# Kernel tuning notes

Hardware: AMD Instinct MI355X
Metric: run time of the kernel (lower is better)

Reference implementation:

```python
import jax, jax.numpy as jnp
import numpy as np

L, B, S, H, NH, NS = 4, 8, 2048, 1024, 2, 32
DH = H // NH


def _ln(x, g, b, eps):
    m = jnp.mean(x, axis=-1, keepdims=True)
    v = jnp.mean((x - m) ** 2, axis=-1, keepdims=True)
    return (x - m) / jnp.sqrt(v + eps) * g + b


def setup_inputs() -> dict:
    key = jax.random.key(0)
    ks = jax.random.split(key, 8)
    sc = 0.02
    hidden_states = jax.random.normal(ks[0], (L, B, S, H), jnp.float32)
    attention_mask = jnp.ones((B, S), jnp.int32)
    bnd = jnp.sort(jax.random.randint(ks[1], (B, NS + 1), 0, S - 1), axis=1)
    span_head_idxs = bnd[:, :-1]
    span_tail_idxs = jnp.maximum(bnd[:, 1:], span_head_idxs + 1)  # tail > head, <= S-... (S-1+1=S ok since slice end)
    return {
        "hidden_states": hidden_states,
        "attention_mask": attention_mask,
        "span_head_idxs": span_head_idxs,
        "span_tail_idxs": span_tail_idxs,
        "layer_weights": jnp.linspace(-5.0, 5.0, L),
        "ln1_g": jnp.ones((H,)), "ln1_b": jnp.zeros((H,)),
        "Wq": jax.random.normal(ks[2], (H, H)) * sc, "bq": jnp.zeros((H,)),
        "Wk": jax.random.normal(ks[3], (H, H)) * sc, "bk": jnp.zeros((H,)),
        "Wv": jax.random.normal(ks[4], (H, H)) * sc, "bv": jnp.zeros((H,)),
        "Wo": jax.random.normal(ks[5], (H, H)) * sc, "bo": jnp.zeros((H,)),
        "ln2_g": jnp.ones((H,)), "ln2_b": jnp.zeros((H,)),
    }


def reference(hidden_states, attention_mask, span_head_idxs, span_tail_idxs,
              layer_weights, ln1_g, ln1_b, Wq, bq, Wk, bk, Wv, bv, Wo, bo,
              ln2_g, ln2_b):
    l, b, s, h = hidden_states.shape
    # weighted layer average
    w = jax.nn.softmax(layer_weights)                      # [L]
    x = jnp.einsum('l,lbsh->bsh', w, hidden_states)        # [B,S,H]
    # extended mask (additive)
    ext = (1.0 - attention_mask.astype(x.dtype))[:, None, None, :] * -10000.0
    x = _ln(x, ln1_g, ln1_b, 1e-7)
    # BertSelfAttention (dropout = identity in eval)
    q = (x @ Wq.T + bq).reshape(b, s, NH, DH)
    k = (x @ Wk.T + bk).reshape(b, s, NH, DH)
    v = (x @ Wv.T + bv).reshape(b, s, NH, DH)
    scores = jnp.einsum('bqnd,bknd->bnqk', q, k) / jnp.sqrt(jnp.asarray(DH, x.dtype))
    probs = jax.nn.softmax(scores + ext, axis=-1)          # [B,NH,S,S]
    ctx = jnp.einsum('bnqk,bknd->bqnd', probs, v).reshape(b, s, h)
    # BertSelfOutput: dense + residual + LN (eps=1e-12 default)
    y = _ln(ctx @ Wo.T + bo + x, ln2_g, ln2_b, 1e-12)      # [B,S,H]
    # ragged per-span mean via exclusive cumsum
    csum = jnp.concatenate([jnp.zeros((b, 1, h), y.dtype), jnp.cumsum(y, axis=1)], axis=1)  # [B,S+1,H]
    sh = jnp.take_along_axis(csum, span_head_idxs[..., None], axis=1)   # [B,NS,H]
    st = jnp.take_along_axis(csum, span_tail_idxs[..., None], axis=1)
    lengths = (span_tail_idxs - span_head_idxs).astype(y.dtype)[..., None]
    return (st - sh) / lengths
```

## Files before the change

kernel.cpp:

```cpp
#include <hip/hip_runtime.h>
#include <stdint.h>

#define Ln 4
#define Bn 8
#define Sn 2048
#define Hn 1024
#define NHn 2
#define DHn 512
#define NSn 32
#define Mn (Bn*Sn)

typedef __attribute__((ext_vector_type(8))) short bf16x8;
typedef __attribute__((ext_vector_type(4))) float f32x4;
typedef unsigned short u16;

__device__ __forceinline__ float bf2f(u16 u){
  union { unsigned int i; float f; } c; c.i = ((unsigned int)u)<<16; return c.f;
}
__device__ __forceinline__ u16 f2bf(float f){
  union { float f; unsigned int i; } c; c.f = f;
  unsigned int r = c.i + 0x7FFFu + ((c.i>>16)&1u);
  return (u16)(r>>16);
}
__device__ __forceinline__ uint32_t packbf(float a, float b){
  return (uint32_t)f2bf(a) | ((uint32_t)f2bf(b)<<16);
}
__device__ __forceinline__ void gl2lds16(const void* g, void* l){
  __builtin_amdgcn_global_load_lds((const __attribute__((address_space(1))) void*)g,
                                   (__attribute__((address_space(3))) void*)l, 16, 0, 0);
}

__device__ __forceinline__ float block_sum256(float v, float* red){
#pragma unroll
  for (int m=32;m>=1;m>>=1) v += __shfl_xor(v, m, 64);
  int tid = threadIdx.x;
  if ((tid&63)==0) red[tid>>6] = v;
  __syncthreads();
  v = red[0]+red[1]+red[2]+red[3];
  __syncthreads();
  return v;
}

__global__ __launch_bounds__(256) void convw_kernel(const float* __restrict__ Wq, const float* __restrict__ Wk,
    const float* __restrict__ Wv, const float* __restrict__ Wo, u16* __restrict__ wb){
  int m = blockIdx.y;
  const float* src = (m==0)?Wq:(m==1)?Wk:(m==2)?Wv:Wo;
  size_t i = ((size_t)blockIdx.x*256 + threadIdx.x)*4;
  const float4 v = *(const float4*)&src[i];
  ushort4 o;
  o.x=f2bf(v.x); o.y=f2bf(v.y); o.z=f2bf(v.z); o.w=f2bf(v.w);
  *(ushort4*)&wb[(size_t)m*Hn*Hn + i] = o;
}

__global__ __launch_bounds__(256) void mixln_kernel(const float* __restrict__ hs, const float* __restrict__ lw,
    const float* __restrict__ g, const float* __restrict__ be, u16* __restrict__ xb){
  __shared__ float red[4];
  int row = blockIdx.x;
  int tid = threadIdx.x;
  float l0=lw[0], l1=lw[1], l2=lw[2], l3=lw[3];
  float mx = fmaxf(fmaxf(l0,l1),fmaxf(l2,l3));
  float e0=__expf(l0-mx), e1=__expf(l1-mx), e2=__expf(l2-mx), e3=__expf(l3-mx);
  float inv = 1.0f/(e0+e1+e2+e3);
  e0*=inv; e1*=inv; e2*=inv; e3*=inv;
  size_t base = (size_t)row*Hn + tid*4;
  const float4 h0 = *(const float4*)&hs[base];
  const float4 h1 = *(const float4*)&hs[base + (size_t)Mn*Hn];
  const float4 h2 = *(const float4*)&hs[base + (size_t)2*Mn*Hn];
  const float4 h3 = *(const float4*)&hs[base + (size_t)3*Mn*Hn];
  float x0 = e0*h0.x + e1*h1.x + e2*h2.x + e3*h3.x;
  float x1 = e0*h0.y + e1*h1.y + e2*h2.y + e3*h3.y;
  float x2 = e0*h0.z + e1*h1.z + e2*h2.z + e3*h3.z;
  float x3 = e0*h0.w + e1*h1.w + e2*h2.w + e3*h3.w;
  float s = block_sum256(x0+x1+x2+x3, red);
  float mean = s * (1.0f/Hn);
  float d0=x0-mean, d1=x1-mean, d2=x2-mean, d3=x3-mean;
  float sq = block_sum256(d0*d0+d1*d1+d2*d2+d3*d3, red);
  float rstd = rsqrtf(sq*(1.0f/Hn) + 1e-7f);
  int c = tid*4;
  ushort4 o;
  o.x = f2bf(d0*rstd*g[c+0] + be[c+0]);
  o.y = f2bf(d1*rstd*g[c+1] + be[c+1]);
  o.z = f2bf(d2*rstd*g[c+2] + be[c+2]);
  o.w = f2bf(d3*rstd*g[c+3] + be[c+3]);
  *(ushort4*)&xb[(size_t)row*Hn + c] = o;
}

template<int MODE>
__global__ __launch_bounds__(512,2) void gemm256_kernel(const u16* __restrict__ A, const u16* __restrict__ Bw,
    const float* __restrict__ bias, const u16* __restrict__ resid, void* __restrict__ Cout, float scale){
  __shared__ char lds[2][2][32768];
  int tid = threadIdx.x, lane = tid&63, wid = tid>>6;
  int ln = lane&15, g4 = lane>>4;
  int wm = wid>>2, wn = wid&3;
  int swz = (blockIdx.x&7)*32 + (blockIdx.x>>3);
  int i0 = (swz>>2)*256;
  int j0 = (swz&3)*256;

  f32x4 acc[8][4];
#pragma unroll
  for (int a=0;a<8;a++)
#pragma unroll
    for (int b=0;b<4;b++) acc[a][b] = (f32x4){0.f,0.f,0.f,0.f};

  const u16* Asrc = A + (size_t)i0*Hn;
  const u16* Bsrc = Bw + (size_t)j0*Hn;

#define STAGE1(SRC, DST, G) do { \
    int g_ = (G); int row_ = g_>>3; int cs_ = (g_&7) ^ (row_&7); \
    gl2lds16((SRC) + (size_t)row_*Hn + cs_*8, (DST) + g_*16); } while(0)

#define RD(BASE, ROW, KG) (*(const bf16x8*)((BASE) + (ROW)*128 + ((((KG)) ^ ((ROW)&7))<<4)))

  {
    const u16* An_ = Asrc; const u16* Bn_ = Bsrc;
#pragma unroll
    for (int c=0;c<4;++c){ STAGE1(An_, lds[0][0], tid + c*512); }
#pragma unroll
    for (int c=0;c<4;++c){ STAGE1(Bn_, lds[0][1], tid + c*512); }
  }
  __syncthreads();

  bf16x8 af[4][2], bf0[2][2], bf1[2][2];

#pragma unroll 1
  for (int t=0; t<16; ++t){
    const char* Ac = lds[t&1][0];
    const char* Bc = lds[t&1][1];
    char* Anx = lds[(t+1)&1][0];
    char* Bnx = lds[(t+1)&1][1];
    const u16* An_ = Asrc + (t+1)*64;
    const u16* Bn_ = Bsrc + (t+1)*64;
    bool st = (t < 15);
    if (st){ STAGE1(An_, Anx, tid); STAGE1(An_, Anx, tid+512); STAGE1(Bn_, Bnx, tid); }
#pragma unroll
    for (int mt=0; mt<4; ++mt)
#pragma unroll
      for (int kk=0; kk<2; ++kk) af[mt][kk] = RD(Ac, wm*128 + mt*16 + ln, kk*4+g4);
#pragma unroll
    for (int nt=0; nt<2; ++nt)
#pragma unroll
      for (int kk=0; kk<2; ++kk) bf0[nt][kk] = RD(Bc, wn*64 + nt*16 + ln, kk*4+g4);
    __builtin_amdgcn_s_barrier();
    __builtin_amdgcn_s_setprio(1);
#pragma unroll
    for (int kk=0; kk<2; ++kk)
#pragma unroll
      for (int mt=0; mt<4; ++mt)
#pragma unroll
        for (int nt=0; nt<2; ++nt)
          acc[mt][nt] = __builtin_amdgcn_mfma_f32_16x16x32_bf16(af[mt][kk], bf0[nt][kk], acc[mt][nt], 0,0,0);
    __builtin_amdgcn_s_setprio(0);
    if (st){ STAGE1(Bn_, Bnx, tid+512); STAGE1(An_, Anx, tid+1024); STAGE1(An_, Anx, tid+1536); }
#pragma unroll
    for (int nt=0; nt<2; ++nt)
#pragma unroll
      for (int kk=0; kk<2; ++kk) bf1[nt][kk] = RD(Bc, wn*64 + (2+nt)*16 + ln, kk*4+g4);
    __builtin_amdgcn_s_barrier();
    __builtin_amdgcn_s_setprio(1);
#pragma unroll
    for (int kk=0; kk<2; ++kk)
#pragma unroll
      for (int mt=0; mt<4; ++mt)
#pragma unroll
        for (int nt=0; nt<2; ++nt)
          acc[mt][2+nt] = __builtin_amdgcn_mfma_f32_16x16x32_bf16(af[mt][kk], bf1[nt][kk], acc[mt][2+nt], 0,0,0);
    __builtin_amdgcn_s_setprio(0);
    if (st){ STAGE1(Bn_, Bnx, tid+1024); STAGE1(Bn_, Bnx, tid+1536); }
#pragma unroll
    for (int mt=0; mt<4; ++mt)
#pragma unroll
      for (int kk=0; kk<2; ++kk) af[mt][kk] = RD(Ac, wm*128 + 64 + mt*16 + ln, kk*4+g4);
    __builtin_amdgcn_s_barrier();
    __builtin_amdgcn_s_setprio(1);
#pragma unroll
    for (int kk=0; kk<2; ++kk)
#pragma unroll
      for (int mt=0; mt<4; ++mt)
#pragma unroll
        for (int nt=0; nt<2; ++nt)
          acc[4+mt][nt] = __builtin_amdgcn_mfma_f32_16x16x32_bf16(af[mt][kk], bf0[nt][kk], acc[4+mt][nt], 0,0,0);
    __builtin_amdgcn_s_setprio(0);
    __builtin_amdgcn_s_barrier();
    __builtin_amdgcn_s_setprio(1);
#pragma unroll
    for (int kk=0; kk<2; ++kk)
#pragma unroll
      for (int mt=0; mt<4; ++mt)
#pragma unroll
        for (int nt=0; nt<2; ++nt)
          acc[4+mt][2+nt] = __builtin_amdgcn_mfma_f32_16x16x32_bf16(af[mt][kk], bf1[nt][kk], acc[4+mt][2+nt], 0,0,0);
    __builtin_amdgcn_s_setprio(0);
    __syncthreads();
  }
#undef STAGE1
#undef RD

#pragma unroll
  for (int mt=0; mt<8; ++mt){
#pragma unroll
    for (int nt=0; nt<4; ++nt){
#pragma unroll
      for (int r=0; r<4; ++r){
        int i = i0 + wm*128 + mt*16 + g4*4 + r;
        int j = j0 + wn*64 + nt*16 + ln;
        float v = acc[mt][nt][r] + bias[j];
        if (MODE==0){
          int b = i>>11, s = i&2047, nh = j>>9, dh = j&511;
          ((u16*)Cout)[(((size_t)(b*NHn+nh)*Sn + s)<<9) + dh] = f2bf(v*scale);
        } else if (MODE==1){
          int b = i>>11, s = i&2047, nh = j>>9, dh = j&511;
          ((u16*)Cout)[((size_t)((b*NHn+nh)*(Sn/32) + (s>>5))<<14) + (dh<<5) + (s&31)] = f2bf(v);
        } else {
          float res = bf2f(resid[(size_t)i*Hn + j]);
          ((float*)Cout)[(size_t)i*Hn + j] = v + res;
        }
      }
    }
  }
}

__global__ __launch_bounds__(512,2) void attn_kernel(const u16* __restrict__ qb, const u16* __restrict__ kb,
    const u16* __restrict__ vt, const int* __restrict__ mask, u16* __restrict__ ctx){
  __shared__ u16 Ks[2][32*512];
  __shared__ u16 Vs[2][512*32];
  __shared__ u16 Ps[8*16*32];
  __shared__ float Lcorr[128];
  __shared__ float Lflag[8];
  __shared__ float Linv[128];
  int tid = threadIdx.x, lane = tid&63, wid = tid>>6;
  int ln = lane&15, g4 = lane>>4;
  int gid = blockIdx.x;
  int xcd = gid&7, ord = gid>>3;
  int bh = xcd*2 + (ord>>4), qt = ord&15;
  int b = bh >> 1, nh = bh & 1;
  u16* pw = Ps + wid*512;
  uint32_t* pw32 = (uint32_t*)pw;
  const int swz = (ln&7)<<4;
  const int rsw = (ln>>1)&3;

  bf16x8 aq[16];
  size_t qoff = ((size_t)bh*Sn + qt*128 + wid*16 + ln)*DHn + g4*8;
#pragma unroll
  for (int ch=0; ch<16; ++ch) aq[ch] = *(const bf16x8*)&qb[qoff + ch*32];

  f32x4 o2[8][4];
#pragma unroll
  for (int qf=0; qf<8; ++qf)
#pragma unroll
    for (int df=0; df<4; ++df) o2[qf][df] = (f32x4){0.f,0.f,0.f,0.f};
  float mrun = -1e30f, lrun = 0.f;

  const size_t kbase = (size_t)bh*Sn*DHn;
  const u16* vtile = vt + (size_t)bh*Sn*DHn;

#define STAGE_KV(KT,BUF) do { \
  _Pragma("unroll") \
  for (int t_=0; t_<4; ++t_){ \
    int krow_ = t_*8 + wid; \
    int koff_ = (lane*16) ^ ((krow_&7)<<4); \
    gl2lds16(&kb[kbase + ((size_t)((KT)*32 + krow_))*DHn + (koff_>>1)], \
             (char*)Ks[BUF] + krow_*1024 + lane*16); \
  } \
  _Pragma("unroll") \
  for (int t_=0; t_<4; ++t_){ \
    int p_ = t_*512 + tid; \
    int cgd_ = ((p_&3) ^ ((p_>>3)&3)); \
    gl2lds16(&vtile[(size_t)(KT)*16384 + (p_&~3)*8 + cgd_*8], \
             (char*)Vs[BUF] + p_*16); \
  } } while(0)

  STAGE_KV(0,0);
  __syncthreads();
#pragma unroll 1
  for (int kt=0; kt<Sn/32; ++kt){
    int cur = kt&1;
    if (kt < Sn/32 - 1) STAGE_KV(kt+1, cur^1);
    const char* KsB = (const char*)Ks[cur];
    f32x4 s0 = (f32x4){0.f,0.f,0.f,0.f};
    f32x4 s1 = (f32x4){0.f,0.f,0.f,0.f};
#pragma unroll
    for (int ch=0; ch<16; ++ch){
      bf16x8 k0 = *(const bf16x8*)(KsB + ln*1024      + ((ch*64 + g4*16) ^ swz));
      bf16x8 k1 = *(const bf16x8*)(KsB + (16+ln)*1024 + ((ch*64 + g4*16) ^ swz));
      s0 = __builtin_amdgcn_mfma_f32_16x16x32_bf16(k0, aq[ch], s0, 0,0,0);
      s1 = __builtin_amdgcn_mfma_f32_16x16x32_bf16(k1, aq[ch], s1, 0,0,0);
    }
    int4 mk0 = *(const int4*)&mask[b*Sn + kt*32 + g4*4];
    int4 mk1 = *(const int4*)&mask[b*Sn + kt*32 + 16 + g4*4];
    s0[0] += (float)(1-mk0.x)*-10000.0f; s0[1] += (float)(1-mk0.y)*-10000.0f;
    s0[2] += (float)(1-mk0.z)*-10000.0f; s0[3] += (float)(1-mk0.w)*-10000.0f;
    s1[0] += (float)(1-mk1.x)*-10000.0f; s1[1] += (float)(1-mk1.y)*-10000.0f;
    s1[2] += (float)(1-mk1.z)*-10000.0f; s1[3] += (float)(1-mk1.w)*-10000.0f;
    float tmax = fmaxf(fmaxf(fmaxf(s0[0],s0[1]),fmaxf(s0[2],s0[3])),
                       fmaxf(fmaxf(s1[0],s1[1]),fmaxf(s1[2],s1[3])));
    tmax = fmaxf(tmax, __shfl_xor(tmax, 16));
    tmax = fmaxf(tmax, __shfl_xor(tmax, 32));
    float corr = 1.0f, wflag = 0.0f;
    if (__any(tmax > mrun + 8.0f)){
      float nm = fmaxf(mrun, tmax);
      corr = __expf(mrun - nm);
      mrun = nm; lrun *= corr;
      wflag = 1.0f;
    }
    float p0=__expf(s0[0]-mrun), p1=__expf(s0[1]-mrun), p2=__expf(s0[2]-mrun), p3=__expf(s0[3]-mrun);
    float p4=__expf(s1[0]-mrun), p5=__expf(s1[1]-mrun), p6=__expf(s1[2]-mrun), p7=__expf(s1[3]-mrun);
    float sum = ((p0+p1)+(p2+p3)) + ((p4+p5)+(p6+p7));
    sum += __shfl_xor(sum, 16);
    sum += __shfl_xor(sum, 32);
    lrun += sum;
    {
      int base = ln*16 + ((g4&1)<<1);
      pw32[base + (((g4>>1)    ^rsw)<<2)    ] = packbf(p0,p1);
      pw32[base + (((g4>>1)    ^rsw)<<2) + 1] = packbf(p2,p3);
      pw32[base + ((((g4>>1)+2)^rsw)<<2)    ] = packbf(p4,p5);
      pw32[base + ((((g4>>1)+2)^rsw)<<2) + 1] = packbf(p6,p7);
    }
    if (lane < 16) Lcorr[wid*16 + ln] = corr;
    if (lane == 0) Lflag[wid] = wflag;
    __builtin_amdgcn_sched_barrier(0);
    asm volatile("s_waitcnt lgkmcnt(0)" ::: "memory");
    __builtin_amdgcn_s_barrier();
    __builtin_amdgcn_sched_barrier(0);
    {
      f32x4 fl0 = *(const f32x4*)&Lflag[0];
      f32x4 fl1 = *(const f32x4*)&Lflag[4];
      float fs = (fl0[0]+fl0[1]+fl0[2]+fl0[3]) + (fl1[0]+fl1[1]+fl1[2]+fl1[3]);
      if (fs > 0.5f){
#pragma unroll
        for (int qf=0; qf<8; ++qf){
          f32x4 c4 = *(const f32x4*)&Lcorr[qf*16 + g4*4];
#pragma unroll
          for (int df=0; df<4; ++df){
            o2[qf][df][0]*=c4[0]; o2[qf][df][1]*=c4[1];
            o2[qf][df][2]*=c4[2]; o2[qf][df][3]*=c4[3];
          }
        }
      }
    }
    const char* VsB = (const char*)Vs[cur];
    bf16x8 bv[4];
#pragma unroll
    for (int df=0; df<4; ++df)
      bv[df] = *(const bf16x8*)(VsB + ((wid*4+df)*16+ln)*64 + ((g4 ^ rsw)<<4));
#pragma unroll
    for (int qf=0; qf<8; ++qf){
      bf16x8 aP = *(const bf16x8*)&Ps[qf*512 + ln*32 + ((g4 ^ rsw)<<3)];
#pragma unroll
      for (int df=0; df<4; ++df)
        o2[qf][df] = __builtin_amdgcn_mfma_f32_16x16x32_bf16(aP, bv[df], o2[qf][df], 0,0,0);
    }
    __syncthreads();
  }
#undef STAGE_KV
  if (lane < 16) Linv[wid*16 + ln] = 1.0f/lrun;
  __syncthreads();
  int qr0 = qt*128;
#pragma unroll
  for (int qf=0; qf<8; ++qf){
    f32x4 il4 = *(const f32x4*)&Linv[qf*16 + g4*4];
#pragma unroll
    for (int df=0; df<4; ++df){
#pragma unroll
      for (int r=0; r<4; ++r){
        int q = qr0 + qf*16 + g4*4 + r;
        int d = nh*DHn + wid*64 + df*16 + ln;
        ctx[((size_t)(b*Sn + q))*Hn + d] = f2bf(o2[qf][df][r]*il4[r]);
      }
    }
  }
}

__global__ __launch_bounds__(256) void ln2_kernel(float* __restrict__ t, const float* __restrict__ g,
    const float* __restrict__ be){
  __shared__ float red[4];
  int row = blockIdx.x, tid = threadIdx.x;
  const float4 x = *(const float4*)&t[(size_t)row*Hn + tid*4];
  float s = block_sum256(x.x+x.y+x.z+x.w, red);
  float mean = s*(1.0f/Hn);
  float d0=x.x-mean, d1=x.y-mean, d2=x.z-mean, d3=x.w-mean;
  float sq = block_sum256(d0*d0+d1*d1+d2*d2+d3*d3, red);
  float rstd = rsqrtf(sq*(1.0f/Hn) + 1e-12f);
  int c = tid*4;
  float4 y;
  y.x = d0*rstd*g[c+0] + be[c+0];
  y.y = d1*rstd*g[c+1] + be[c+1];
  y.z = d2*rstd*g[c+2] + be[c+2];
  y.w = d3*rstd*g[c+3] + be[c+3];
  *(float4*)&t[(size_t)row*Hn + c] = y;
}

__global__ __launch_bounds__(256) void span_kernel(const float* __restrict__ y, const int* __restrict__ head,
    const int* __restrict__ tail, float* __restrict__ out){
  int bs = blockIdx.x;
  int b = bs >> 5;
  int hd = head[bs], tl = tail[bs];
  int c = threadIdx.x*4;
  float a0=0.f,a1=0.f,a2=0.f,a3=0.f;
  for (int s=hd; s<tl; ++s){
    const float4 v = *(const float4*)&y[((size_t)(b*Sn + s))*Hn + c];
    a0+=v.x; a1+=v.y; a2+=v.z; a3+=v.w;
  }
  float inv = 1.0f/(float)(tl-hd);
  float4 o; o.x=a0*inv; o.y=a1*inv; o.z=a2*inv; o.w=a3*inv;
  *(float4*)&out[(size_t)bs*Hn + c] = o;
}

extern "C" void kernel_launch(void* const* d_in, const int* in_sizes, int n_in,
                              void* d_out, int out_size, void* d_ws, size_t ws_size,
                              hipStream_t stream) {
  const float* hs    = (const float*)d_in[0];
  const int*   mask  = (const int*)d_in[1];
  const int*   shead = (const int*)d_in[2];
  const int*   stail = (const int*)d_in[3];
  const float* lw    = (const float*)d_in[4];
  const float* ln1g  = (const float*)d_in[5];
  const float* ln1b  = (const float*)d_in[6];
  const float* Wq    = (const float*)d_in[7];
  const float* bq    = (const float*)d_in[8];
  const float* Wk    = (const float*)d_in[9];
  const float* bk    = (const float*)d_in[10];
  const float* Wv    = (const float*)d_in[11];
  const float* bv    = (const float*)d_in[12];
  const float* Wo    = (const float*)d_in[13];
  const float* bo    = (const float*)d_in[14];
  const float* ln2g  = (const float*)d_in[15];
  const float* ln2b  = (const float*)d_in[16];

  char* ws = (char*)d_ws;
  u16* xb  = (u16*)(ws);
  u16* wb  = (u16*)(ws + 33554432);
  u16* qb  = (u16*)(ws + 41943040);
  u16* kb  = (u16*)(ws + 75497472);
  u16* vt  = (u16*)(ws + 109051904);
  u16* ctx = (u16*)(ws + 142606336);
  float* t = (float*)(ws + 41943040);
  float* out = (float*)d_out;

  convw_kernel<<<dim3(1024,4),256,0,stream>>>(Wq,Wk,Wv,Wo,wb);
  mixln_kernel<<<Mn,256,0,stream>>>(hs,lw,ln1g,ln1b,xb);
  gemm256_kernel<0><<<256,512,0,stream>>>(xb, wb,           bq, nullptr, qb, 0.044194173824159223f);
  gemm256_kernel<0><<<256,512,0,stream>>>(xb, wb+1048576,   bk, nullptr, kb, 1.0f);
  gemm256_kernel<1><<<256,512,0,stream>>>(xb, wb+2097152,   bv, nullptr, vt, 1.0f);
  attn_kernel<<<256,512,0,stream>>>(qb,kb,vt,mask,ctx);
  gemm256_kernel<2><<<256,512,0,stream>>>(ctx, wb+3145728,  bo, xb, t, 1.0f);
  ln2_kernel<<<Mn,256,0,stream>>>(t, ln2g, ln2b);
  span_kernel<<<Bn*NSn,256,0,stream>>>(t, shead, stail, out);
}
```

Measured before the change: 548.2 us.

## Shrink attention block to 64 queries and read V straight from global

The attention kernel now runs 512 blocks of 256 threads, each handling 64 query rows instead of 128. V is no longer staged through LDS. Each wave loads its 128-column slice of the blocked V layout directly into registers, split into two batches placed around the QK MFMA loop to hide latency. This cuts LDS use and the V staging traffic and raises block count, but halves K reuse per block and doubles global K reads, while the per-wave V loads go straight to global/L2 memory.

New measurement: 1.308 ms. 2.39x slower.

```diff
diff --git a/kernel.cpp b/kernel.cpp
--- a/kernel.cpp
+++ b/kernel.cpp
@@ -219,19 +219,18 @@
   }
 }
 
-__global__ __launch_bounds__(512,2) void attn_kernel(const u16* __restrict__ qb, const u16* __restrict__ kb,
+__global__ __launch_bounds__(256,2) void attn_kernel(const u16* __restrict__ qb, const u16* __restrict__ kb,
     const u16* __restrict__ vt, const int* __restrict__ mask, u16* __restrict__ ctx){
   __shared__ u16 Ks[2][32*512];
-  __shared__ u16 Vs[2][512*32];
-  __shared__ u16 Ps[8*16*32];
-  __shared__ float Lcorr[128];
-  __shared__ float Lflag[8];
-  __shared__ float Linv[128];
+  __shared__ u16 Ps[4*16*32];
+  __shared__ float Lcorr[64];
+  __shared__ float Lflag[4];
+  __shared__ float Linv[64];
   int tid = threadIdx.x, lane = tid&63, wid = tid>>6;
   int ln = lane&15, g4 = lane>>4;
   int gid = blockIdx.x;
   int xcd = gid&7, ord = gid>>3;
-  int bh = xcd*2 + (ord>>4), qt = ord&15;
+  int bh = xcd*2 + (ord>>5), qt = ord&31;
   int b = bh >> 1, nh = bh & 1;
   u16* pw = Ps + wid*512;
   uint32_t* pw32 = (uint32_t*)pw;
@@ -239,42 +238,39 @@
   const int rsw = (ln>>1)&3;
 
   bf16x8 aq[16];
-  size_t qoff = ((size_t)bh*Sn + qt*128 + wid*16 + ln)*DHn + g4*8;
+  size_t qoff = ((size_t)bh*Sn + qt*64 + wid*16 + ln)*DHn + g4*8;
 #pragma unroll
   for (int ch=0; ch<16; ++ch) aq[ch] = *(const bf16x8*)&qb[qoff + ch*32];
 
-  f32x4 o2[8][4];
-#pragma unroll
-  for (int qf=0; qf<8; ++qf)
-#pragma unroll
-    for (int df=0; df<4; ++df) o2[qf][df] = (f32x4){0.f,0.f,0.f,0.f};
+  f32x4 o2[4][8];
+#pragma unroll
+  for (int qf=0; qf<4; ++qf)
+#pragma unroll
+    for (int df=0; df<8; ++df) o2[qf][df] = (f32x4){0.f,0.f,0.f,0.f};
   float mrun = -1e30f, lrun = 0.f;
 
   const size_t kbase = (size_t)bh*Sn*DHn;
-  const u16* vtile = vt + (size_t)bh*Sn*DHn;
-
-#define STAGE_KV(KT,BUF) do { \
+  const u16* vbase = vt + (size_t)bh*Sn*DHn + (wid*128 + ln)*32 + g4*8;
+
+#define STAGE_K(KT,BUF) do { \
   _Pragma("unroll") \
-  for (int t_=0; t_<4; ++t_){ \
-    int krow_ = t_*8 + wid; \
+  for (int t_=0; t_<8; ++t_){ \
+    int krow_ = t_*4 + wid; \
     int koff_ = (lane*16) ^ ((krow_&7)<<4); \
     gl2lds16(&kb[kbase + ((size_t)((KT)*32 + krow_))*DHn + (koff_>>1)], \
              (char*)Ks[BUF] + krow_*1024 + lane*16); \
-  } \
-  _Pragma("unroll") \
-  for (int t_=0; t_<4; ++t_){ \
-    int p_ = t_*512 + tid; \
-    int cgd_ = ((p_&3) ^ ((p_>>3)&3)); \
-    gl2lds16(&vtile[(size_t)(KT)*16384 + (p_&~3)*8 + cgd_*8], \
-             (char*)Vs[BUF] + p_*16); \
   } } while(0)
 
-  STAGE_KV(0,0);
+  STAGE_K(0,0);
   __syncthreads();
 #pragma unroll 1
   for (int kt=0; kt<Sn/32; ++kt){
     int cur = kt&1;
-    if (kt < Sn/32 - 1) STAGE_KV(kt+1, cur^1);
+    if (kt < Sn/32 - 1) STAGE_K(kt+1, cur^1);
+    const u16* vkt = vbase + kt*16384;
+    bf16x8 vf[8];
+#pragma unroll
+    for (int df=0; df<4; ++df) vf[df] = *(const bf16x8*)(vkt + df*512);
     const char* KsB = (const char*)Ks[cur];
     f32x4 s0 = (f32x4){0.f,0.f,0.f,0.f};
     f32x4 s1 = (f32x4){0.f,0.f,0.f,0.f};
@@ -285,6 +281,8 @@
       s0 = __builtin_amdgcn_mfma_f32_16x16x32_bf16(k0, aq[ch], s0, 0,0,0);
       s1 = __builtin_amdgcn_mfma_f32_16x16x32_bf16(k1, aq[ch], s1, 0,0,0);
     }
+#pragma unroll
+    for (int df=4; df<8; ++df) vf[df] = *(const bf16x8*)(vkt + df*512);
     int4 mk0 = *(const int4*)&mask[b*Sn + kt*32 + g4*4];
     int4 mk1 = *(const int4*)&mask[b*Sn + kt*32 + 16 + g4*4];
     s0[0] += (float)(1-mk0.x)*-10000.0f; s0[1] += (float)(1-mk0.y)*-10000.0f;
@@ -322,48 +320,42 @@
     __builtin_amdgcn_s_barrier();
     __builtin_amdgcn_sched_barrier(0);
     {
-      f32x4 fl0 = *(const f32x4*)&Lflag[0];
-      f32x4 fl1 = *(const f32x4*)&Lflag[4];
-      float fs = (fl0[0]+fl0[1]+fl0[2]+fl0[3]) + (fl1[0]+fl1[1]+fl1[2]+fl1[3]);
+      f32x4 fl = *(const f32x4*)&Lflag[0];
+      float fs = (fl[0]+fl[1])+(fl[2]+fl[3]);
       if (fs > 0.5f){
 #pragma unroll
-        for (int qf=0; qf<8; ++qf){
+        for (int qf=0; qf<4; ++qf){
           f32x4 c4 = *(const f32x4*)&Lcorr[qf*16 + g4*4];
 #pragma unroll
-          for (int df=0; df<4; ++df){
+          for (int df=0; df<8; ++df){
             o2[qf][df][0]*=c4[0]; o2[qf][df][1]*=c4[1];
             o2[qf][df][2]*=c4[2]; o2[qf][df][3]*=c4[3];
           }
         }
       }
     }
-    const char* VsB = (const char*)Vs[cur];
-    bf16x8 bv[4];
-#pragma unroll
-    for (int df=0; df<4; ++df)
-      bv[df] = *(const bf16x8*)(VsB + ((wid*4+df)*16+ln)*64 + ((g4 ^ rsw)<<4));
-#pragma unroll
-    for (int qf=0; qf<8; ++qf){
+#pragma unroll
+    for (int qf=0; qf<4; ++qf){
       bf16x8 aP = *(const bf16x8*)&Ps[qf*512 + ln*32 + ((g4 ^ rsw)<<3)];
 #pragma unroll
-      for (int df=0; df<4; ++df)
-        o2[qf][df] = __builtin_amdgcn_mfma_f32_16x16x32_bf16(aP, bv[df], o2[qf][df], 0,0,0);
+      for (int df=0; df<8; ++df)
+        o2[qf][df] = __builtin_amdgcn_mfma_f32_16x16x32_bf16(aP, vf[df], o2[qf][df], 0,0,0);
     }
     __syncthreads();
   }
-#undef STAGE_KV
+#undef STAGE_K
   if (lane < 16) Linv[wid*16 + ln] = 1.0f/lrun;
   __syncthreads();
-  int qr0 = qt*128;
-#pragma unroll
-  for (int qf=0; qf<8; ++qf){
+  int qr0 = qt*64;
+#pragma unroll
+  for (int qf=0; qf<4; ++qf){
     f32x4 il4 = *(const f32x4*)&Linv[qf*16 + g4*4];
 #pragma unroll
-    for (int df=0; df<4; ++df){
+    for (int df=0; df<8; ++df){
 #pragma unroll
       for (int r=0; r<4; ++r){
         int q = qr0 + qf*16 + g4*4 + r;
-        int d = nh*DHn + wid*64 + df*16 + ln;
+        int d = nh*DHn + wid*128 + df*16 + ln;
         ctx[((size_t)(b*Sn + q))*Hn + d] = f2bf(o2[qf][df][r]*il4[r]);
       }
     }
@@ -441,7 +433,7 @@
   gemm256_kernel<0><<<256,512,0,stream>>>(xb, wb,           bq, nullptr, qb, 0.044194173824159223f);
   gemm256_kernel<0><<<256,512,0,stream>>>(xb, wb+1048576,   bk, nullptr, kb, 1.0f);
   gemm256_kernel<1><<<256,512,0,stream>>>(xb, wb+2097152,   bv, nullptr, vt, 1.0f);
-  attn_kernel<<<256,512,0,stream>>>(qb,kb,vt,mask,ctx);
+  attn_kernel<<<512,256,0,stream>>>(qb,kb,vt,mask,ctx);
   gemm256_kernel<2><<<256,512,0,stream>>>(ctx, wb+3145728,  bo, xb, t, 1.0f);
   ln2_kernel<<<Mn,256,0,stream>>>(t, ln2g, ln2b);
   span_kernel<<<Bn*NSn,256,0,stream>>>(t, shead, stail, out);
```

## Use triple-buffered K=32 LDS pipeline with explicit waitcnt in GEMM kernel

Applied to the files above, without the earlier changes.

Replaces the double-buffered K=64 LDS pipeline in the 256x256 GEMM with a triple-buffered K=32 scheme that prefetches two tiles ahead. Each iteration does one batch of LDS reads and 32 MFMAs, with a single barrier guarded by explicit vmcnt waits instead of several interleaved barriers per iteration. The aim is to hide global-load latency better and cut barrier overhead. In exchange it doubles the iteration count, uses a narrower swizzle that may raise bank conflicts, and holds more fragment registers live at once.

Measured after the change: 604.3 us. 10.2% more time.

```diff
diff --git a/kernel.cpp b/kernel.cpp
--- a/kernel.cpp
+++ b/kernel.cpp
@@ -88,7 +88,8 @@
 template<int MODE>
 __global__ __launch_bounds__(512,2) void gemm256_kernel(const u16* __restrict__ A, const u16* __restrict__ Bw,
     const float* __restrict__ bias, const u16* __restrict__ resid, void* __restrict__ Cout, float scale){
-  __shared__ char lds[2][2][32768];
+  __shared__ u16 Asb[3][256*32];
+  __shared__ u16 Bsb[3][256*32];
   int tid = threadIdx.x, lane = tid&63, wid = tid>>6;
   int ln = lane&15, g4 = lane>>4;
   int wm = wid>>2, wn = wid&3;
@@ -105,95 +106,51 @@
   const u16* Asrc = A + (size_t)i0*Hn;
   const u16* Bsrc = Bw + (size_t)j0*Hn;
 
-#define STAGE1(SRC, DST, G) do { \
-    int g_ = (G); int row_ = g_>>3; int cs_ = (g_&7) ^ (row_&7); \
-    gl2lds16((SRC) + (size_t)row_*Hn + cs_*8, (DST) + g_*16); } while(0)
-
-#define RD(BASE, ROW, KG) (*(const bf16x8*)((BASE) + (ROW)*128 + ((((KG)) ^ ((ROW)&7))<<4)))
-
-  {
-    const u16* An_ = Asrc; const u16* Bn_ = Bsrc;
-#pragma unroll
-    for (int c=0;c<4;++c){ STAGE1(An_, lds[0][0], tid + c*512); }
-#pragma unroll
-    for (int c=0;c<4;++c){ STAGE1(Bn_, lds[0][1], tid + c*512); }
+#define STG(T,I) do { \
+  _Pragma("unroll") \
+  for (int c_=0;c_<2;++c_){ \
+    int g_ = tid + c_*512; int r_ = g_>>2; int cs_ = (g_&3) ^ (r_&3); \
+    gl2lds16(Asrc + (size_t)r_*Hn + (T)*32 + cs_*8, (char*)Asb[I] + g_*16); \
+    gl2lds16(Bsrc + (size_t)r_*Hn + (T)*32 + cs_*8, (char*)Bsb[I] + g_*16); \
+  } } while(0)
+
+#define RDA(I,ROW) (*(const bf16x8*)((char*)Asb[I] + (ROW)*64 + ((g4 ^ ((ROW)&3))<<4)))
+#define RDB(I,ROW) (*(const bf16x8*)((char*)Bsb[I] + (ROW)*64 + ((g4 ^ ((ROW)&3))<<4)))
+
+  STG(0,0);
+  STG(1,1);
+  asm volatile("s_waitcnt vmcnt(4)" ::: "memory");
+  __builtin_amdgcn_s_barrier();
+  __builtin_amdgcn_sched_barrier(0);
+
+#pragma unroll 1
+  for (int t=0; t<32; ++t){
+    int cur = t%3;
+    if (t < 30) STG(t+2, (t+2)%3);
+    bf16x8 af[8], bf[4];
+#pragma unroll
+    for (int mt=0; mt<8; ++mt) af[mt] = RDA(cur, wm*128 + mt*16 + ln);
+#pragma unroll
+    for (int nt=0; nt<4; ++nt) bf[nt] = RDB(cur, wn*64 + nt*16 + ln);
+    asm volatile("s_waitcnt lgkmcnt(0)" ::: "memory");
+    __builtin_amdgcn_sched_barrier(0);
+    __builtin_amdgcn_s_setprio(1);
+#pragma unroll
+    for (int mt=0; mt<8; ++mt)
+#pragma unroll
+      for (int nt=0; nt<4; ++nt)
+        acc[mt][nt] = __builtin_amdgcn_mfma_f32_16x16x32_bf16(af[mt], bf[nt], acc[mt][nt], 0,0,0);
+    __builtin_amdgcn_s_setprio(0);
+    if (t < 31){
+      if (t < 30) asm volatile("s_waitcnt vmcnt(4)" ::: "memory");
+      else        asm volatile("s_waitcnt vmcnt(0)" ::: "memory");
+      __builtin_amdgcn_s_barrier();
+      __builtin_amdgcn_sched_barrier(0);
+    }
   }
-  __syncthreads();
-
-  bf16x8 af[4][2], bf0[2][2], bf1[2][2];
-
-#pragma unroll 1
-  for (int t=0; t<16; ++t){
-    const char* Ac = lds[t&1][0];
-    const char* Bc = lds[t&1][1];
-    char* Anx = lds[(t+1)&1][0];
-    char* Bnx = lds[(t+1)&1][1];
-    const u16* An_ = Asrc + (t+1)*64;
-    const u16* Bn_ = Bsrc + (t+1)*64;
-    bool st = (t < 15);
-    if (st){ STAGE1(An_, Anx, tid); STAGE1(An_, Anx, tid+512); STAGE1(Bn_, Bnx, tid); }
-#pragma unroll
-    for (int mt=0; mt<4; ++mt)
-#pragma unroll
-      for (int kk=0; kk<2; ++kk) af[mt][kk] = RD(Ac, wm*128 + mt*16 + ln, kk*4+g4);
-#pragma unroll
-    for (int nt=0; nt<2; ++nt)
-#pragma unroll
-      for (int kk=0; kk<2; ++kk) bf0[nt][kk] = RD(Bc, wn*64 + nt*16 + ln, kk*4+g4);
-    __builtin_amdgcn_s_barrier();
-    __builtin_amdgcn_s_setprio(1);
-#pragma unroll
-    for (int kk=0; kk<2; ++kk)
-#pragma unroll
-      for (int mt=0; mt<4; ++mt)
-#pragma unroll
-        for (int nt=0; nt<2; ++nt)
-          acc[mt][nt] = __builtin_amdgcn_mfma_f32_16x16x32_bf16(af[mt][kk], bf0[nt][kk], acc[mt][nt], 0,0,0);
-    __builtin_amdgcn_s_setprio(0);
-    if (st){ STAGE1(Bn_, Bnx, tid+512); STAGE1(An_, Anx, tid+1024); STAGE1(An_, Anx, tid+1536); }
-#pragma unroll
-    for (int nt=0; nt<2; ++nt)
-#pragma unroll
-      for (int kk=0; kk<2; ++kk) bf1[nt][kk] = RD(Bc, wn*64 + (2+nt)*16 + ln, kk*4+g4);
-    __builtin_amdgcn_s_barrier();
-    __builtin_amdgcn_s_setprio(1);
-#pragma unroll
-    for (int kk=0; kk<2; ++kk)
-#pragma unroll
-      for (int mt=0; mt<4; ++mt)
-#pragma unroll
-        for (int nt=0; nt<2; ++nt)
-          acc[mt][2+nt] = __builtin_amdgcn_mfma_f32_16x16x32_bf16(af[mt][kk], bf1[nt][kk], acc[mt][2+nt], 0,0,0);
-    __builtin_amdgcn_s_setprio(0);
-    if (st){ STAGE1(Bn_, Bnx, tid+1024); STAGE1(Bn_, Bnx, tid+1536); }
-#pragma unroll
-    for (int mt=0; mt<4; ++mt)
-#pragma unroll
-      for (int kk=0; kk<2; ++kk) af[mt][kk] = RD(Ac, wm*128 + 64 + mt*16 + ln, kk*4+g4);
-    __builtin_amdgcn_s_barrier();
-    __builtin_amdgcn_s_setprio(1);
-#pragma unroll
-    for (int kk=0; kk<2; ++kk)
-#pragma unroll
-      for (int mt=0; mt<4; ++mt)
-#pragma unroll
-        for (int nt=0; nt<2; ++nt)
-          acc[4+mt][nt] = __builtin_amdgcn_mfma_f32_16x16x32_bf16(af[mt][kk], bf0[nt][kk], acc[4+mt][nt], 0,0,0);
-    __builtin_amdgcn_s_setprio(0);
-    __builtin_amdgcn_s_barrier();
-    __builtin_amdgcn_s_setprio(1);
-#pragma unroll
-    for (int kk=0; kk<2; ++kk)
-#pragma unroll
-      for (int mt=0; mt<4; ++mt)
-#pragma unroll
-        for (int nt=0; nt<2; ++nt)
-          acc[4+mt][2+nt] = __builtin_amdgcn_mfma_f32_16x16x32_bf16(af[mt][kk], bf1[nt][kk], acc[4+mt][2+nt], 0,0,0);
-    __builtin_amdgcn_s_setprio(0);
-    __syncthreads();
-  }
-#undef STAGE1
-#undef RD
+#undef STG
+#undef RDA
+#undef RDB
 
 #pragma unroll
   for (int mt=0; mt<8; ++mt){
```
